# Optimization experiments

Measured on AMD Instinct MI355X. Metric: run time of the kernel, lower is better.

Reference implementation:

```python
import jax, jax.numpy as jnp
import numpy as np

KEY_IN = 256
QUERY_IN = 256
KEY_CH = 32
HEADS = 8
VAL_CH = 64
DK = KEY_CH // HEADS   # 4
DV = VAL_CH // HEADS   # 8
SCALE = DK ** -0.5


def _conv1x1(x, w, b):
    # x: [B,C,H,W], w: [O,C], b: [O] -> [B,O,H,W]
    return jnp.einsum('bchw,oc->bohw', x, w) + b[None, :, None, None]


def setup_inputs() -> dict:
    key = jax.random.key(0)
    ks = jax.random.split(key, 10)
    B, H, W = 8, 128, 128
    target = jax.random.normal(ks[0], (B, QUERY_IN, H, W), dtype=jnp.float32)
    inp = jax.random.normal(ks[1], (B, KEY_IN, H, W), dtype=jnp.float32)
    s = 0.02
    return {
        'target': target,
        'input': inp,
        'kw': jax.random.normal(ks[2], (KEY_CH, KEY_IN), dtype=jnp.float32) * s,
        'kb': jnp.zeros((KEY_CH,), dtype=jnp.float32),
        'qw': jax.random.normal(ks[3], (KEY_CH, QUERY_IN), dtype=jnp.float32) * s,
        'qb': jnp.zeros((KEY_CH,), dtype=jnp.float32),
        'vw': jax.random.normal(ks[4], (VAL_CH, KEY_IN), dtype=jnp.float32) * s,
        'vb': jnp.zeros((VAL_CH,), dtype=jnp.float32),
        'rw': jax.random.normal(ks[5], (QUERY_IN, VAL_CH), dtype=jnp.float32) * s,
        'rb': jnp.zeros((QUERY_IN,), dtype=jnp.float32),
    }


def reference(target, input, kw, kb, qw, qb, vw, vb, rw, rb):
    B, _, H, W = input.shape
    HW = H * W
    k = _conv1x1(input, kw, kb).reshape(B, HEADS, DK, HW)
    q = _conv1x1(target, qw, qb).reshape(B, HEADS, DK, HW)
    v = _conv1x1(input, vw, vb).reshape(B, HEADS, DV, HW)
    k = jax.nn.softmax(k, axis=-1)            # softmax over spatial positions
    q = jax.nn.softmax(q * SCALE, axis=-2)    # softmax over key-channel dim
    context = jnp.einsum('bhdn,bhen->bhde', k, v)   # [B,H,DK,DV]
    out = jnp.einsum('bhde,bhdn->bhen', context, q) # [B,H,DV,HW]
    out = out.reshape(B, VAL_CH, H, W)
    return _conv1x1(out, rw, rb)
```

## Files before the change

kernel.cpp:

```cpp
#include <hip/hip_runtime.h>
#include <hip/hip_bf16.h>
#include <math.h>

#define BATCH 8
#define HW 16384
#define CIN 256
#define KCH 32
#define VCH 64
#define HEADS 8
#define DK 4
#define DV 8
#define SCALE 0.5f

typedef _Float16 f16;
typedef f16 f16x8 __attribute__((ext_vector_type(8)));
typedef float f32x4 __attribute__((ext_vector_type(4)));

#define WS_WKVF 0
#define WS_QWF  12288
#define WS_RWF  16384
#define WS_KP   24576
#define WS_VP   (WS_KP + BATCH*16*HW)
#define WS_PART (WS_VP + BATCH*32*HW)
#define WS_CTX  (WS_PART + BATCH*HEADS*16*40)

__device__ inline unsigned pack_bf16(float a, float b) {
    unsigned ua = __float_as_uint(a);
    unsigned ub = __float_as_uint(b);
    ua = (ua + 0x7fffu + ((ua >> 16) & 1u)) >> 16;
    ub = (ub + 0x7fffu + ((ub >> 16) & 1u)) >> 16;
    return ua | (ub << 16);
}
__device__ inline float2 unpack_bf16(unsigned u) {
    float2 r;
    r.x = __uint_as_float(u << 16);
    r.y = __uint_as_float(u & 0xffff0000u);
    return r;
}
__device__ inline unsigned pk_f16(float a, float b) {
    auto h = __builtin_amdgcn_cvt_pkrtz(a, b);
    union { decltype(h) v; unsigned u; } c;
    c.v = h;
    return c.u;
}

__global__ void prepack(const float* __restrict__ kw, const float* __restrict__ vw,
                        const float* __restrict__ qw, const float* __restrict__ rw,
                        f16* __restrict__ wkvf, f16* __restrict__ qwf, f16* __restrict__ rwf) {
    int t = blockIdx.x * 256 + threadIdx.x;
    int stride = gridDim.x * 256;
    for (int i = t; i < 6*8*64*8; i += stride) {
        int j = i & 7, lane = (i >> 3) & 63, kc = (i >> 9) & 7, mt = i >> 12;
        int row = mt*16 + (lane & 15);
        int k = kc*32 + (lane >> 4)*8 + j;
        float v = row < 32 ? kw[row*CIN + k] : vw[(row-32)*CIN + k];
        wkvf[i] = (f16)v;
    }
    for (int i = t; i < 2*8*64*8; i += stride) {
        int j = i & 7, lane = (i >> 3) & 63, kc = (i >> 9) & 7, mt = i >> 12;
        int row = mt*16 + (lane & 15);
        int k = kc*32 + (lane >> 4)*8 + j;
        qwf[i] = (f16)qw[row*CIN + k];
    }
    for (int i = t; i < 16*2*64*8; i += stride) {
        int j = i & 7, lane = (i >> 3) & 63, kc2 = (i >> 9) & 1, mt = i >> 10;
        int row = mt*16 + (lane & 15);
        int e = kc2*32 + (lane >> 4)*8 + j;
        rwf[i] = (f16)rw[row*VCH + e];
    }
}

__global__ void __launch_bounds__(256) proj_kv_mfma(const float* __restrict__ x,
    const f16* __restrict__ wkvf, const float* __restrict__ kb_,
    const float* __restrict__ vb_, unsigned* __restrict__ kp_out,
    unsigned* __restrict__ vp_out) {
    int b    = blockIdx.x >> 7;
    int bpx  = (blockIdx.x & 127) * 128;
    int wave = threadIdx.x >> 6, lane = threadIdx.x & 63;
    int wm = wave >> 1, wn = wave & 1;
    int col = lane & 15, kb = lane >> 4;
    int px0 = bpx + wn * 64;
    const float* Xb = x + (size_t)b * CIN * HW;

    f32x4 acc[3][4];
#pragma unroll
    for (int m = 0; m < 3; ++m)
#pragma unroll
        for (int n = 0; n < 4; ++n) acc[m][n] = (f32x4){0.f, 0.f, 0.f, 0.f};

    for (int kc = 0; kc < 8; ++kc) {
        f16x8 afr[3];
#pragma unroll
        for (int mt = 0; mt < 3; ++mt)
            afr[mt] = *(const f16x8*)(wkvf + (size_t)(((wm*3 + mt)*8 + kc)*64 + lane)*8);
        float xb[4][8];
#pragma unroll
        for (int nt = 0; nt < 4; ++nt)
#pragma unroll
            for (int j = 0; j < 8; ++j)
                xb[nt][j] = Xb[(size_t)(kc*32 + kb*8 + j)*HW + px0 + nt*16 + col];
        f16x8 bfr[4];
#pragma unroll
        for (int nt = 0; nt < 4; ++nt) {
            union { f16x8 v; unsigned u[4]; } u;
#pragma unroll
            for (int p = 0; p < 4; ++p)
                u.u[p] = pk_f16(xb[nt][2*p], xb[nt][2*p+1]);
            bfr[nt] = u.v;
        }
#pragma unroll
        for (int mt = 0; mt < 3; ++mt)
#pragma unroll
            for (int nt = 0; nt < 4; ++nt)
                acc[mt][nt] = __builtin_amdgcn_mfma_f32_16x16x32_f16(
                    afr[mt], bfr[nt], acc[mt][nt], 0, 0, 0);
    }

#pragma unroll
    for (int mt = 0; mt < 3; ++mt) {
        int row0 = wm*48 + mt*16 + kb*4;
        bool isk = row0 < 32;
        float4 bias = isk ? *(const float4*)(kb_ + row0)
                          : *(const float4*)(vb_ + row0 - 32);
#pragma unroll
        for (int nt = 0; nt < 4; ++nt) {
            int px = px0 + nt*16 + col;
            float v0 = acc[mt][nt][0] + bias.x;
            float v1 = acc[mt][nt][1] + bias.y;
            float v2 = acc[mt][nt][2] + bias.z;
            float v3 = acc[mt][nt][3] + bias.w;
            if (isk) {
                unsigned* kp = kp_out + (size_t)(b*16 + (row0 >> 1))*HW + px;
                kp[0]  = pack_bf16(expf(v0), expf(v1));
                kp[HW] = pack_bf16(expf(v2), expf(v3));
            } else {
                int vr = row0 - 32;
                unsigned* vp = vp_out + (size_t)(b*32 + (vr >> 1))*HW + px;
                vp[0]  = pack_bf16(v0, v1);
                vp[HW] = pack_bf16(v2, v3);
            }
        }
    }
}

__global__ void __launch_bounds__(256) ctx_partial(const unsigned* __restrict__ kp_in,
                                                   const unsigned* __restrict__ vp_in,
                                                   float* __restrict__ part) {
    int blk = blockIdx.x;
    int b  = blk >> 7;
    int h  = (blk >> 4) & 7;
    int ch = blk & 15;
    const unsigned* kp = kp_in + (size_t)b * 16 * HW + (size_t)(2*h) * HW;
    const unsigned* vp = vp_in + (size_t)b * 32 * HW + (size_t)(4*h) * HW;

    float den[DK] = {0.f, 0.f, 0.f, 0.f};
    float num[DK][DV] = {};

    int n0 = ch * 1024 + threadIdx.x;
#pragma unroll
    for (int it = 0; it < 4; ++it) {
        int n = n0 + it * 256;
        unsigned ku0 = kp[n], ku1 = kp[HW + n];
        unsigned vu0 = vp[n], vu1 = vp[HW + n];
        unsigned vu2 = vp[2*HW + n], vu3 = vp[3*HW + n];
        float2 k01 = unpack_bf16(ku0), k23 = unpack_bf16(ku1);
        float ek[DK] = {k01.x, k01.y, k23.x, k23.y};
        float2 va = unpack_bf16(vu0), vb2 = unpack_bf16(vu1);
        float2 vc = unpack_bf16(vu2), vd = unpack_bf16(vu3);
        float vv[DV] = {va.x, va.y, vb2.x, vb2.y, vc.x, vc.y, vd.x, vd.y};
#pragma unroll
        for (int d = 0; d < DK; ++d) {
            den[d] += ek[d];
#pragma unroll
            for (int e = 0; e < DV; ++e) num[d][e] += ek[d] * vv[e];
        }
    }

    __shared__ float red[36][4];
    int lane = threadIdx.x & 63;
    int wv   = threadIdx.x >> 6;
#pragma unroll
    for (int i = 0; i < 36; ++i) {
        float val = (i < 4) ? den[i] : num[(i - 4) >> 3][(i - 4) & 7];
        for (int off = 32; off; off >>= 1) val += __shfl_down(val, off);
        if (lane == 0) red[i][wv] = val;
    }
    __syncthreads();
    if (threadIdx.x < 36) {
        float s = red[threadIdx.x][0] + red[threadIdx.x][1] +
                  red[threadIdx.x][2] + red[threadIdx.x][3];
        part[(size_t)blk * 40 + threadIdx.x] = s;
    }
}

__global__ void ctx_final(const float* __restrict__ part,
                          float* __restrict__ ctx) {
    int b = blockIdx.x;
    int t = threadIdx.x;
    int h = t >> 5, d = (t >> 3) & 3, e = t & 7;
    float num = 0.f, den = 0.f;
#pragma unroll
    for (int ch = 0; ch < 16; ++ch) {
        const float* pp = part + (size_t)(((b * 8 + h) * 16 + ch)) * 40;
        num += pp[4 + d * 8 + e];
        den += pp[d];
    }
    ctx[(((size_t)b * 8 + h) * 8 + e) * 4 + d] = num / den;
}

#define FNT 2
__global__ void __launch_bounds__(256) fused_mfma(const float* __restrict__ tgt,
    const f16* __restrict__ qwf, const float* __restrict__ qb_,
    const float* __restrict__ ctx, const f16* __restrict__ rwf,
    const float* __restrict__ rb_, float* __restrict__ out) {
    int b    = blockIdx.x >> 7;
    int bpx  = (blockIdx.x & 127) * 128;
    int wave = threadIdx.x >> 6, lane = threadIdx.x & 63;
    int col = lane & 15, kb = lane >> 4;
    int px0 = bpx + wave * (FNT * 16);
    const float* Tb = tgt + (size_t)b * CIN * HW;

    f32x4 qacc[2][FNT];
#pragma unroll
    for (int m = 0; m < 2; ++m)
#pragma unroll
        for (int n = 0; n < FNT; ++n) qacc[m][n] = (f32x4){0.f, 0.f, 0.f, 0.f};

    for (int kc = 0; kc < 8; ++kc) {
        f16x8 afr[2];
#pragma unroll
        for (int mt = 0; mt < 2; ++mt)
            afr[mt] = *(const f16x8*)(qwf + (size_t)((mt*8 + kc)*64 + lane)*8);
        float xb[FNT][8];
#pragma unroll
        for (int nt = 0; nt < FNT; ++nt)
#pragma unroll
            for (int j = 0; j < 8; ++j)
                xb[nt][j] = Tb[(size_t)(kc*32 + kb*8 + j)*HW + px0 + nt*16 + col];
        f16x8 bfr[FNT];
#pragma unroll
        for (int nt = 0; nt < FNT; ++nt) {
            union { f16x8 v; unsigned u[4]; } u;
#pragma unroll
            for (int p = 0; p < 4; ++p)
                u.u[p] = pk_f16(xb[nt][2*p], xb[nt][2*p+1]);
            bfr[nt] = u.v;
        }
#pragma unroll
        for (int mt = 0; mt < 2; ++mt)
#pragma unroll
            for (int nt = 0; nt < FNT; ++nt)
                qacc[mt][nt] = __builtin_amdgcn_mfma_f32_16x16x32_f16(
                    afr[mt], bfr[nt], qacc[mt][nt], 0, 0, 0);
    }

    unsigned attnu[2][FNT][4];
#pragma unroll
    for (int mt2 = 0; mt2 < 2; ++mt2) {
        int h = mt2*4 + kb;
        float4 qb4 = *(const float4*)(qb_ + mt2*16 + kb*4);
        float4 cx[8];
#pragma unroll
        for (int e = 0; e < 8; ++e)
            cx[e] = *(const float4*)(ctx + (size_t)((b*8 + h)*8 + e)*4);
#pragma unroll
        for (int nt = 0; nt < FNT; ++nt) {
            float s0 = (qacc[mt2][nt][0] + qb4.x) * SCALE;
            float s1 = (qacc[mt2][nt][1] + qb4.y) * SCALE;
            float s2 = (qacc[mt2][nt][2] + qb4.z) * SCALE;
            float s3 = (qacc[mt2][nt][3] + qb4.w) * SCALE;
            float m  = fmaxf(fmaxf(s0, s1), fmaxf(s2, s3));
            float e0 = expf(s0 - m), e1 = expf(s1 - m);
            float e2 = expf(s2 - m), e3 = expf(s3 - m);
            float inv = 1.f / (e0 + e1 + e2 + e3);
            float w0 = e0*inv, w1 = e1*inv, w2 = e2*inv, w3 = e3*inv;
            float at[8];
#pragma unroll
            for (int e = 0; e < 8; ++e)
                at[e] = cx[e].x*w0 + cx[e].y*w1 + cx[e].z*w2 + cx[e].w*w3;
#pragma unroll
            for (int p = 0; p < 4; ++p)
                attnu[mt2][nt][p] = pk_f16(at[2*p], at[2*p+1]);
        }
    }

    float* Ob = out + (size_t)b * CIN * HW;
    for (int pm = 0; pm < 4; ++pm) {
        f32x4 oacc[4][FNT];
#pragma unroll
        for (int m = 0; m < 4; ++m)
#pragma unroll
            for (int n = 0; n < FNT; ++n) oacc[m][n] = (f32x4){0.f, 0.f, 0.f, 0.f};
#pragma unroll
        for (int kc2 = 0; kc2 < 2; ++kc2) {
            f16x8 bfr2[FNT];
#pragma unroll
            for (int nt = 0; nt < FNT; ++nt) {
                union { f16x8 v; unsigned u[4]; } c;
#pragma unroll
                for (int p = 0; p < 4; ++p) c.u[p] = attnu[kc2][nt][p];
                bfr2[nt] = c.v;
            }
#pragma unroll
            for (int mt = 0; mt < 4; ++mt) {
                f16x8 afr2 = *(const f16x8*)(rwf +
                    (size_t)((((pm*4 + mt)*2 + kc2)*64 + lane))*8);
#pragma unroll
                for (int nt = 0; nt < FNT; ++nt)
                    oacc[mt][nt] = __builtin_amdgcn_mfma_f32_16x16x32_f16(
                        afr2, bfr2[nt], oacc[mt][nt], 0, 0, 0);
            }
        }
#pragma unroll
        for (int mt = 0; mt < 4; ++mt) {
            int o0 = (pm*4 + mt)*16 + kb*4;
            float4 rb4 = *(const float4*)(rb_ + o0);
#pragma unroll
            for (int nt = 0; nt < FNT; ++nt) {
                int px = px0 + nt*16 + col;
                float* op = Ob + (size_t)o0 * HW + px;
                op[0]              = oacc[mt][nt][0] + rb4.x;
                op[HW]             = oacc[mt][nt][1] + rb4.y;
                op[2*(size_t)HW]   = oacc[mt][nt][2] + rb4.z;
                op[3*(size_t)HW]   = oacc[mt][nt][3] + rb4.w;
            }
        }
    }
}

extern "C" void kernel_launch(void* const* d_in, const int* in_sizes, int n_in,
                              void* d_out, int out_size, void* d_ws, size_t ws_size,
                              hipStream_t stream) {
    const float* target = (const float*)d_in[0];
    const float* input  = (const float*)d_in[1];
    const float* kw = (const float*)d_in[2];
    const float* kb = (const float*)d_in[3];
    const float* qw = (const float*)d_in[4];
    const float* qb = (const float*)d_in[5];
    const float* vw = (const float*)d_in[6];
    const float* vb = (const float*)d_in[7];
    const float* rw = (const float*)d_in[8];
    const float* rb = (const float*)d_in[9];
    float* out = (float*)d_out;
    float* ws  = (float*)d_ws;

    f16*      wkvf = (f16*)(ws + WS_WKVF);
    f16*      qwf  = (f16*)(ws + WS_QWF);
    f16*      rwf  = (f16*)(ws + WS_RWF);
    unsigned* kp   = (unsigned*)(ws + WS_KP);
    unsigned* vp   = (unsigned*)(ws + WS_VP);
    float*    part = ws + WS_PART;
    float*    ctx  = ws + WS_CTX;

    hipLaunchKernelGGL(prepack, dim3(32), dim3(256), 0, stream,
                       kw, vw, qw, rw, wkvf, qwf, rwf);
    hipLaunchKernelGGL(proj_kv_mfma, dim3(BATCH * HW / 128), dim3(256), 0, stream,
                       input, wkvf, kb, vb, kp, vp);
    hipLaunchKernelGGL(ctx_partial, dim3(BATCH * HEADS * 16), dim3(256), 0, stream,
                       kp, vp, part);
    hipLaunchKernelGGL(ctx_final, dim3(BATCH), dim3(256), 0, stream,
                       part, ctx);
    hipLaunchKernelGGL(fused_mfma, dim3(BATCH * HW / 128), dim3(256), 0, stream,
                       target, qwf, qb, ctx, rwf, rb, out);
}
```

Before: 132.9 us.

## Stage target tiles via async LDS loads and transpose output MFMA for float4 stores

The target activations are now double-buffered in shared memory with global_load_lds. Each block loads a coalesced 32-channel by 128-pixel tile for the next k-chunk while MFMAs run on the current one, instead of every lane doing strided scalar global loads. The output projection MFMA swaps its operands so the accumulator rows are pixels. Each lane can then write a contiguous float4 instead of four scattered scalar stores. The cost is 32 KB of LDS per block, which may lower occupancy, and two barriers per k-iteration.

```diff
diff --git a/kernel.cpp b/kernel.cpp
--- a/kernel.cpp
+++ b/kernel.cpp
@@ -43,6 +43,10 @@
     c.v = h;
     return c.u;
 }
+
+#define GLDS16(g, l) __builtin_amdgcn_global_load_lds( \
+    (__attribute__((address_space(1))) const void*)(g), \
+    (__attribute__((address_space(3))) void*)(l), 16, 0, 0)
 
 __global__ void prepack(const float* __restrict__ kw, const float* __restrict__ vw,
                         const float* __restrict__ qw, const float* __restrict__ rw,
@@ -213,13 +217,20 @@
     const f16* __restrict__ qwf, const float* __restrict__ qb_,
     const float* __restrict__ ctx, const f16* __restrict__ rwf,
     const float* __restrict__ rb_, float* __restrict__ out) {
+    __shared__ float tile[2][4096];
     int b    = blockIdx.x >> 7;
-    int bpx  = (blockIdx.x & 127) * 128;
+    int pxb  = (blockIdx.x & 127) * 128;
     int wave = threadIdx.x >> 6, lane = threadIdx.x & 63;
     int col = lane & 15, kb = lane >> 4;
-    int px0 = bpx + wave * (FNT * 16);
     const float* Tb = tgt + (size_t)b * CIN * HW;
 
+    int c0   = wave*8 + (lane >> 5);
+    int px_g = pxb + (lane & 31)*4;
+
+#pragma unroll
+    for (int i = 0; i < 4; ++i)
+        GLDS16(Tb + (size_t)(c0 + i*2)*HW + px_g, &tile[0][wave*1024 + i*256]);
+
     f32x4 qacc[2][FNT];
 #pragma unroll
     for (int m = 0; m < 2; ++m)
@@ -227,23 +238,29 @@
         for (int n = 0; n < FNT; ++n) qacc[m][n] = (f32x4){0.f, 0.f, 0.f, 0.f};
 
     for (int kc = 0; kc < 8; ++kc) {
+        int cur = kc & 1;
+        __syncthreads();
+        if (kc < 7) {
+#pragma unroll
+            for (int i = 0; i < 4; ++i)
+                GLDS16(Tb + (size_t)((kc+1)*32 + c0 + i*2)*HW + px_g,
+                       &tile[cur ^ 1][wave*1024 + i*256]);
+        }
         f16x8 afr[2];
 #pragma unroll
         for (int mt = 0; mt < 2; ++mt)
             afr[mt] = *(const f16x8*)(qwf + (size_t)((mt*8 + kc)*64 + lane)*8);
-        float xb[FNT][8];
-#pragma unroll
-        for (int nt = 0; nt < FNT; ++nt)
-#pragma unroll
-            for (int j = 0; j < 8; ++j)
-                xb[nt][j] = Tb[(size_t)(kc*32 + kb*8 + j)*HW + px0 + nt*16 + col];
         f16x8 bfr[FNT];
 #pragma unroll
         for (int nt = 0; nt < FNT; ++nt) {
+            const float* tp = &tile[cur][kb*1024 + wave*32 + nt*16 + col];
+            float x[8];
+#pragma unroll
+            for (int j = 0; j < 8; ++j) x[j] = tp[j*128];
             union { f16x8 v; unsigned u[4]; } u;
 #pragma unroll
             for (int p = 0; p < 4; ++p)
-                u.u[p] = pk_f16(xb[nt][2*p], xb[nt][2*p+1]);
+                u.u[p] = pk_f16(x[2*p], x[2*p+1]);
             bfr[nt] = u.v;
         }
 #pragma unroll
@@ -252,6 +269,7 @@
             for (int nt = 0; nt < FNT; ++nt)
                 qacc[mt][nt] = __builtin_amdgcn_mfma_f32_16x16x32_f16(
                     afr[mt], bfr[nt], qacc[mt][nt], 0, 0, 0);
+        __syncthreads();
     }
 
     unsigned attnu[2][FNT][4];
@@ -286,43 +304,41 @@
 
     float* Ob = out + (size_t)b * CIN * HW;
     for (int pm = 0; pm < 4; ++pm) {
-        f32x4 oacc[4][FNT];
-#pragma unroll
-        for (int m = 0; m < 4; ++m)
-#pragma unroll
-            for (int n = 0; n < FNT; ++n) oacc[m][n] = (f32x4){0.f, 0.f, 0.f, 0.f};
+        f32x4 oacc[FNT][4];
+#pragma unroll
+        for (int n = 0; n < FNT; ++n)
+#pragma unroll
+            for (int m = 0; m < 4; ++m) oacc[n][m] = (f32x4){0.f, 0.f, 0.f, 0.f};
 #pragma unroll
         for (int kc2 = 0; kc2 < 2; ++kc2) {
-            f16x8 bfr2[FNT];
+            f16x8 afr2[FNT];
 #pragma unroll
             for (int nt = 0; nt < FNT; ++nt) {
                 union { f16x8 v; unsigned u[4]; } c;
 #pragma unroll
                 for (int p = 0; p < 4; ++p) c.u[p] = attnu[kc2][nt][p];
-                bfr2[nt] = c.v;
+                afr2[nt] = c.v;
             }
 #pragma unroll
-            for (int mt = 0; mt < 4; ++mt) {
-                f16x8 afr2 = *(const f16x8*)(rwf +
-                    (size_t)((((pm*4 + mt)*2 + kc2)*64 + lane))*8);
+            for (int ot = 0; ot < 4; ++ot) {
+                f16x8 bfr2 = *(const f16x8*)(rwf +
+                    (size_t)((((pm*4 + ot)*2 + kc2)*64 + lane))*8);
 #pragma unroll
                 for (int nt = 0; nt < FNT; ++nt)
-                    oacc[mt][nt] = __builtin_amdgcn_mfma_f32_16x16x32_f16(
-                        afr2, bfr2[nt], oacc[mt][nt], 0, 0, 0);
+                    oacc[nt][ot] = __builtin_amdgcn_mfma_f32_16x16x32_f16(
+                        afr2[nt], bfr2, oacc[nt][ot], 0, 0, 0);
             }
         }
 #pragma unroll
-        for (int mt = 0; mt < 4; ++mt) {
-            int o0 = (pm*4 + mt)*16 + kb*4;
-            float4 rb4 = *(const float4*)(rb_ + o0);
+        for (int ot = 0; ot < 4; ++ot) {
+            int o = (pm*4 + ot)*16 + col;
+            float rbv = rb_[o];
 #pragma unroll
             for (int nt = 0; nt < FNT; ++nt) {
-                int px = px0 + nt*16 + col;
-                float* op = Ob + (size_t)o0 * HW + px;
-                op[0]              = oacc[mt][nt][0] + rb4.x;
-                op[HW]             = oacc[mt][nt][1] + rb4.y;
-                op[2*(size_t)HW]   = oacc[mt][nt][2] + rb4.z;
-                op[3*(size_t)HW]   = oacc[mt][nt][3] + rb4.w;
+                int px = pxb + wave*32 + nt*16 + kb*4;
+                float4 st = { oacc[nt][ot][0] + rbv, oacc[nt][ot][1] + rbv,
+                              oacc[nt][ot][2] + rbv, oacc[nt][ot][3] + rbv };
+                *(float4*)(Ob + (size_t)o * HW + px) = st;
             }
         }
     }
```

After: 130.2 us. -2.0%, faster.
